# Optimization experiments

Hardware: AMD Instinct MI355X
Metric: run time of the kernel (lower is better)

## Reference

```python
import jax, jax.numpy as jnp
import numpy as np
from jax import lax

B, C, H, W = 32, 256, 56, 56
OUT_C, K, M = 256, 3, 8
STRIDE = (1, 1)
PADDING = ((1, 1), (1, 1))


def setup_inputs() -> dict:
    key = jax.random.key(0)
    ks = jax.random.split(key, 5)
    x = jax.random.normal(ks[0], (B, C, H, W), dtype=jnp.float32)
    # expert kernels: (M, out_C, in_C/groups, kh, kw), init like torch.randn*0.02
    weight = jax.random.normal(ks[1], (M, OUT_C, C, K, K), dtype=jnp.float32) * 0.02
    bias = jnp.zeros((M, OUT_C), dtype=jnp.float32)
    # gate Linear(in=C, out=M): torch stores weight as (out, in)
    bound = 1.0 / np.sqrt(C)
    gate_w = jax.random.uniform(ks[2], (M, C), minval=-bound, maxval=bound, dtype=jnp.float32)
    gate_b = jax.random.uniform(ks[3], (M,), minval=-bound, maxval=bound, dtype=jnp.float32)
    return {"x": x, "weight": weight, "bias": bias, "gate_w": gate_w, "gate_b": gate_b}


def reference(x, weight, bias, gate_w, gate_b):
    # global average pool -> gating
    gap = jnp.mean(x, axis=(2, 3))                         # (B, C)
    alpha = jax.nn.softmax(gap @ gate_w.T + gate_b, axis=1)  # (B, M)
    # per-sample combined kernels and biases
    kernels = jnp.einsum('bm,moikl->boikl', alpha, weight)  # (B, O, I, k, k)
    biases = alpha @ bias                                   # (B, O)

    def conv_one(xi, wi):
        # xi: (C,H,W), wi: (O,I,k,k)
        out = lax.conv_general_dilated(
            xi[None], wi,
            window_strides=STRIDE, padding=PADDING,
            dimension_numbers=('NCHW', 'OIHW', 'NCHW'))
        return out[0]  # (O, H, W)

    out = jax.vmap(conv_one)(x, kernels)                    # (B, O, H, W)
    return out + biases[:, :, None, None]
```

## Files before the change

### kernel.cpp

```cpp
#include <hip/hip_runtime.h>
#include <hip/hip_bf16.h>

#define B_    32
#define C_    256
#define HW_   3136
#define OC_   256
#define M_    8
#define KPB_  589824

typedef short v8s __attribute__((ext_vector_type(8)));
typedef float f32x4 __attribute__((ext_vector_type(4)));

union bf8pack { v8s v; __hip_bfloat16 h[8]; };

__device__ __forceinline__ void gll16(const short* src, short* dst) {
    __builtin_amdgcn_global_load_lds((const __attribute__((address_space(1))) void*)src,
                                     (__attribute__((address_space(3))) void*)dst, 16, 0, 0);
}

__global__ void zero_gap_kernel(float* __restrict__ gap) {
    gap[blockIdx.x * 256 + threadIdx.x] = 0.f;
}

__global__ __launch_bounds__(256) void xcast_kernel(const float* __restrict__ x,
                                                    short* __restrict__ xg,
                                                    float* __restrict__ gap) {
    __shared__ __hip_bfloat16 tile[64][65];
    int b = blockIdx.z, ct = blockIdx.y, pt = blockIdx.x;
    int p0 = pt*64, c0 = ct*64;
    int tp = threadIdx.x & 63, tc = threadIdx.x >> 6;
    const float* xb = x + ((size_t)b*C_ + c0) * HW_ + p0;
    #pragma unroll
    for (int j = 0; j < 16; ++j) {
        int cl = tc + j*4;
        float v = xb[(size_t)cl*HW_ + tp];
        tile[cl][tp] = __float2bfloat16(v);
        float s = v;
        #pragma unroll
        for (int off = 32; off; off >>= 1) s += __shfl_xor(s, off, 64);
        if (tp == 0) atomicAdd(&gap[b*C_ + c0 + cl], s);
    }
    __syncthreads();
    #pragma unroll
    for (int it = 0; it < 2; ++it) {
        int idx = it*256 + threadIdx.x;
        int px = idx >> 3, ck = idx & 7;
        bf8pack pk;
        #pragma unroll
        for (int j = 0; j < 8; ++j) pk.h[j] = tile[ck*8 + j][px];
        int c = c0 + ck*8;
        size_t dst = (((size_t)b*8 + (c >> 5))*HW_ + p0 + px)*32 + (c & 31);
        *(v8s*)(xg + dst) = pk.v;
    }
}

__global__ void alpha_kernel(const float* __restrict__ gap,
                             const float* __restrict__ gate_w,
                             const float* __restrict__ gate_b,
                             const float* __restrict__ bias,
                             float* __restrict__ alpha,
                             float* __restrict__ biasc) {
    int b = blockIdx.x, lane = threadIdx.x;
    const float inv = 1.0f / HW_;
    float g0 = gap[b*C_ + lane]*inv,       g1 = gap[b*C_ + 64 + lane]*inv;
    float g2 = gap[b*C_ + 128 + lane]*inv, g3 = gap[b*C_ + 192 + lane]*inv;
    float logit[M_];
    #pragma unroll
    for (int m = 0; m < M_; ++m) {
        const float* w = gate_w + m*C_;
        float s = g0*w[lane] + g1*w[64+lane] + g2*w[128+lane] + g3*w[192+lane];
        for (int off = 32; off; off >>= 1) s += __shfl_xor(s, off, 64);
        logit[m] = s + gate_b[m];
    }
    float mx = logit[0];
    #pragma unroll
    for (int m = 1; m < M_; ++m) mx = fmaxf(mx, logit[m]);
    float den = 0.f, e[M_];
    #pragma unroll
    for (int m = 0; m < M_; ++m) { e[m] = __expf(logit[m] - mx); den += e[m]; }
    float am[M_];
    #pragma unroll
    for (int m = 0; m < M_; ++m) am[m] = e[m] / den;
    if (lane < M_) alpha[b*M_ + lane] = am[lane];
    #pragma unroll
    for (int r = 0; r < 4; ++r) {
        int o = r*64 + lane;
        float s = 0.f;
        #pragma unroll
        for (int m = 0; m < M_; ++m) s += am[m] * bias[m*OC_ + o];
        biasc[b*OC_ + o] = s;
    }
}

__global__ __launch_bounds__(256) void combine_kernel(const float* __restrict__ weight,
                                                      const float* __restrict__ alpha,
                                                      short* __restrict__ wl) {
    __shared__ float as[B_*M_];
    as[threadIdx.x] = alpha[threadIdx.x];
    __syncthreads();
    int gc  = blockIdx.x*256 + threadIdx.x;
    int i8  = gc & 3;
    int o   = (gc >> 2) & 255;
    int t2  = gc >> 10;
    int tap = t2 % 9;
    int ib  = t2 / 9;
    int base = o*2304 + (ib*32 + i8*8)*9 + tap;
    float wv[M_][8];
    #pragma unroll
    for (int m = 0; m < M_; ++m)
        #pragma unroll
        for (int j = 0; j < 8; ++j)
            wv[m][j] = weight[(size_t)m*589824 + base + j*9];
    for (int b = 0; b < B_; ++b) {
        bf8pack pk;
        #pragma unroll
        for (int j = 0; j < 8; ++j) {
            float s = 0.f;
            #pragma unroll
            for (int m = 0; m < M_; ++m) s += as[b*M_+m] * wv[m][j];
            pk.h[j] = __float2bfloat16(s);
        }
        *(v8s*)(wl + (size_t)b*KPB_ + (size_t)gc*8) = pk.v;
    }
}

__global__ __launch_bounds__(256, 2) void conv_kernel(const short* __restrict__ xg,
                                                      const short* __restrict__ wl,
                                                      const float* __restrict__ biasc,
                                                      float* __restrict__ out) {
    __shared__ short smem[36864];

    const int wg  = blockIdx.x;
    const int swz = (wg & 7) * 104 + (wg >> 3);
    const int b   = swz / 26;
    const int rm  = swz - b * 26;
    const int ot  = rm / 13;
    const int pt  = rm - ot * 13;

    const int tid = threadIdx.x;
    const int wave = tid >> 6, lane = tid & 63, q = lane >> 4, ln = lane & 15;
    const int o_half = wave >> 1, p_half = wave & 1;
    const int P0 = pt*256;

    const int DOFF[9] = {-57,-56,-55,-1,0,1,55,56,57};

    unsigned vmask[8]; int p_lane[8];
    #pragma unroll
    for (int c = 0; c < 8; ++c) {
        int p = P0 + p_half*128 + c*16 + ln;
        p_lane[c] = p;
        int h = p/56, w = p%56;
        unsigned m = 0;
        #pragma unroll
        for (int tap = 0; tap < 9; ++tap) {
            int h2 = h + tap/3 - 1, w2 = w + tap%3 - 1;
            if ((unsigned)h2 < 56u && (unsigned)w2 < 56u) m |= (1u << tap);
        }
        vmask[c] = m;
    }

    const short* wbase = wl + (size_t)b*KPB_ + ot*4096 + tid*8;
    const short* xbase = xg + (size_t)(b*8)*HW_*32;

    auto stageA = [&](int kidx, int buf) {
        const short* src = wbase + (size_t)kidx*8192;
        gll16(src,        &smem[buf*4096 + tid*8]);
        gll16(src + 2048, &smem[buf*4096 + tid*8 + 2048]);
    };
    auto stageB = [&](int ib, int buf) {
        const short* src = xbase + ((long)ib*HW_ + P0 - 64)*32 + tid*8;
        short* dst = &smem[12288 + buf*12288 + tid*8];
        #pragma unroll
        for (int r = 0; r < 6; ++r) gll16(src + r*2048, dst + r*2048);
    };

    f32x4 acc[4][8];
    #pragma unroll
    for (int r = 0; r < 4; ++r)
        #pragma unroll
        for (int c = 0; c < 8; ++c) acc[r][c] = (f32x4){0.f,0.f,0.f,0.f};

    stageB(0, 0);
    stageA(0, 0);
    stageA(1, 1);

    const int a_lane_off = (o_half*64 + ln)*32 + q*8;
    const int b_lane_off = 12288 + (64 + p_half*128 + ln)*32 + q*8;
    const v8s vzero = {};

    for (int ib = 0; ib < 8; ++ib) {
        const short* bbuf = &smem[(ib & 1)*12288 + b_lane_off];
        #pragma unroll
        for (int tap = 0; tap < 9; ++tap) {
            const int k = ib*9 + tap;

            if (k == 71) {
                asm volatile("s_waitcnt vmcnt(0)" ::: "memory");
            } else if ((tap == 1 || tap == 2) && ib < 7) {
                asm volatile("s_waitcnt vmcnt(8)" ::: "memory");
            } else {
                asm volatile("s_waitcnt vmcnt(2)" ::: "memory");
            }
            __builtin_amdgcn_s_barrier();
            asm volatile("" ::: "memory");
            __builtin_amdgcn_sched_barrier(0);

            if (k + 2 < 72) stageA(k + 2, (tap + 2) % 3);
            if (tap == 0 && ib < 7) stageB(ib + 1, (ib + 1) & 1);

            const short* am = &smem[(tap % 3)*4096 + a_lane_off];
            v8s a[4];
            #pragma unroll
            for (int r = 0; r < 4; ++r) a[r] = *(const v8s*)(am + r*512);
            const short* bm = bbuf + DOFF[tap]*32;
            __builtin_amdgcn_s_setprio(1);
            #pragma unroll
            for (int c = 0; c < 8; ++c) {
                v8s v = *(const v8s*)(bm + c*512);
                v8s bf = ((vmask[c] >> tap) & 1) ? v : vzero;
                #pragma unroll
                for (int r = 0; r < 4; ++r)
                    acc[r][c] = __builtin_amdgcn_mfma_f32_16x16x32_bf16(a[r], bf, acc[r][c], 0, 0, 0);
            }
            __builtin_amdgcn_s_setprio(0);
        }
    }

    const int o_block = ot*128 + o_half*64;
    #pragma unroll
    for (int c = 0; c < 8; ++c) {
        int p = p_lane[c];
        if (p >= HW_) continue;
        float* op = out + (size_t)b * OC_ * HW_ + p;
        #pragma unroll
        for (int r = 0; r < 4; ++r) {
            int o0 = o_block + r*16 + q*4;
            #pragma unroll
            for (int reg = 0; reg < 4; ++reg) {
                int o = o0 + reg;
                op[(size_t)o * HW_] = acc[r][c][reg] + biasc[b*OC_ + o];
            }
        }
    }
}

extern "C" void kernel_launch(void* const* d_in, const int* in_sizes, int n_in,
                              void* d_out, int out_size, void* d_ws, size_t ws_size,
                              hipStream_t stream) {
    const float* x      = (const float*)d_in[0];
    const float* weight = (const float*)d_in[1];
    const float* bias   = (const float*)d_in[2];
    const float* gate_w = (const float*)d_in[3];
    const float* gate_b = (const float*)d_in[4];
    float* out = (float*)d_out;

    char* ws = (char*)d_ws;
    float* gap   = (float*)(ws);
    float* biasc = (float*)(ws + 32768);
    float* alpha = (float*)(ws + 65536);
    short* xg    = (short*)(ws + 131072);
    short* wl    = (short*)(ws + 51511296);

    zero_gap_kernel<<<32, 256, 0, stream>>>(gap);
    xcast_kernel   <<<dim3(49, 4, 32), 256, 0, stream>>>(x, xg, gap);
    alpha_kernel   <<<32,  64, 0, stream>>>(gap, gate_w, gate_b, bias, alpha, biasc);
    combine_kernel <<<288, 256, 0, stream>>>(weight, alpha, wl);
    conv_kernel    <<<832, 256, 0, stream>>>(xg, wl, biasc, out);
}
```

Measured before the change: 391.0 us.

## Enlarge conv tile to full 256 output channels by 224 pixels, split combine over batch

Each conv workgroup now covers all 256 output channels and 224 pixels (four pixel rows), where it used to cover 128 channels and 256 pixels. Weight reuse per staged input tile goes up, the padding waste at the end of the pixel range disappears, and the grid drops from 832 to 448 blocks with 1 block per CU. The combine kernel is also split across a second grid dimension over batch groups to add parallelism. In exchange, the larger accumulator array (56 f32x4) raises register pressure, occupancy is lower, and the wait counts were retuned by hand for the new load counts.

```diff
diff --git a/kernel.cpp b/kernel.cpp
--- a/kernel.cpp
+++ b/kernel.cpp
@@ -111,7 +111,8 @@
         #pragma unroll
         for (int j = 0; j < 8; ++j)
             wv[m][j] = weight[(size_t)m*589824 + base + j*9];
-    for (int b = 0; b < B_; ++b) {
+    int b0 = blockIdx.y * 8;
+    for (int b = b0; b < b0 + 8; ++b) {
         bf8pack pk;
         #pragma unroll
         for (int j = 0; j < 8; ++j) {
@@ -124,31 +125,27 @@
     }
 }
 
-__global__ __launch_bounds__(256, 2) void conv_kernel(const short* __restrict__ xg,
+__global__ __launch_bounds__(256, 1) void conv_kernel(const short* __restrict__ xg,
                                                       const short* __restrict__ wl,
                                                       const float* __restrict__ biasc,
                                                       float* __restrict__ out) {
-    __shared__ short smem[36864];
+    __shared__ short smem[49152];
 
     const int wg  = blockIdx.x;
-    const int swz = (wg & 7) * 104 + (wg >> 3);
-    const int b   = swz / 26;
-    const int rm  = swz - b * 26;
-    const int ot  = rm / 13;
-    const int pt  = rm - ot * 13;
+    const int swz = (wg & 7) * 56 + (wg >> 3);
+    const int b   = swz / 14;
+    const int pt  = swz - b * 14;
 
     const int tid = threadIdx.x;
     const int wave = tid >> 6, lane = tid & 63, q = lane >> 4, ln = lane & 15;
-    const int o_half = wave >> 1, p_half = wave & 1;
-    const int P0 = pt*256;
+    const int P0 = pt * 224;
 
     const int DOFF[9] = {-57,-56,-55,-1,0,1,55,56,57};
 
-    unsigned vmask[8]; int p_lane[8];
-    #pragma unroll
-    for (int c = 0; c < 8; ++c) {
-        int p = P0 + p_half*128 + c*16 + ln;
-        p_lane[c] = p;
+    unsigned vmask[14];
+    #pragma unroll
+    for (int c = 0; c < 14; ++c) {
+        int p = P0 + c*16 + ln;
         int h = p/56, w = p%56;
         unsigned m = 0;
         #pragma unroll
@@ -159,33 +156,34 @@
         vmask[c] = m;
     }
 
-    const short* wbase = wl + (size_t)b*KPB_ + ot*4096 + tid*8;
+    const short* wbase = wl + (size_t)b*KPB_ + tid*8;
     const short* xbase = xg + (size_t)(b*8)*HW_*32;
 
     auto stageA = [&](int kidx, int buf) {
         const short* src = wbase + (size_t)kidx*8192;
-        gll16(src,        &smem[buf*4096 + tid*8]);
-        gll16(src + 2048, &smem[buf*4096 + tid*8 + 2048]);
+        #pragma unroll
+        for (int r = 0; r < 4; ++r)
+            gll16(src + r*2048, &smem[buf*8192 + tid*8 + r*2048]);
     };
     auto stageB = [&](int ib, int buf) {
         const short* src = xbase + ((long)ib*HW_ + P0 - 64)*32 + tid*8;
-        short* dst = &smem[12288 + buf*12288 + tid*8];
+        short* dst = &smem[24576 + buf*12288 + tid*8];
         #pragma unroll
         for (int r = 0; r < 6; ++r) gll16(src + r*2048, dst + r*2048);
     };
 
-    f32x4 acc[4][8];
+    f32x4 acc[4][14];
     #pragma unroll
     for (int r = 0; r < 4; ++r)
         #pragma unroll
-        for (int c = 0; c < 8; ++c) acc[r][c] = (f32x4){0.f,0.f,0.f,0.f};
+        for (int c = 0; c < 14; ++c) acc[r][c] = (f32x4){0.f,0.f,0.f,0.f};
 
     stageB(0, 0);
     stageA(0, 0);
     stageA(1, 1);
 
-    const int a_lane_off = (o_half*64 + ln)*32 + q*8;
-    const int b_lane_off = 12288 + (64 + p_half*128 + ln)*32 + q*8;
+    const int a_lane_off = (wave*64 + ln)*32 + q*8;
+    const int b_lane_off = 24576 + (64 + ln)*32 + q*8;
     const v8s vzero = {};
 
     for (int ib = 0; ib < 8; ++ib) {
@@ -196,48 +194,44 @@
 
             if (k == 71) {
                 asm volatile("s_waitcnt vmcnt(0)" ::: "memory");
-            } else if ((tap == 1 || tap == 2) && ib < 7) {
-                asm volatile("s_waitcnt vmcnt(8)" ::: "memory");
+            } else if ((tap == 1 || tap == 2) && k <= 56) {
+                asm volatile("s_waitcnt vmcnt(10)" ::: "memory");
             } else {
-                asm volatile("s_waitcnt vmcnt(2)" ::: "memory");
+                asm volatile("s_waitcnt vmcnt(4)" ::: "memory");
             }
             __builtin_amdgcn_s_barrier();
             asm volatile("" ::: "memory");
             __builtin_amdgcn_sched_barrier(0);
 
-            if (k + 2 < 72) stageA(k + 2, (tap + 2) % 3);
+            if (k + 2 < 72) stageA(k + 2, (k + 2) % 3);
             if (tap == 0 && ib < 7) stageB(ib + 1, (ib + 1) & 1);
 
-            const short* am = &smem[(tap % 3)*4096 + a_lane_off];
+            const short* am = &smem[(k % 3)*8192 + a_lane_off];
             v8s a[4];
             #pragma unroll
             for (int r = 0; r < 4; ++r) a[r] = *(const v8s*)(am + r*512);
             const short* bm = bbuf + DOFF[tap]*32;
-            __builtin_amdgcn_s_setprio(1);
-            #pragma unroll
-            for (int c = 0; c < 8; ++c) {
+            #pragma unroll
+            for (int c = 0; c < 14; ++c) {
                 v8s v = *(const v8s*)(bm + c*512);
                 v8s bf = ((vmask[c] >> tap) & 1) ? v : vzero;
                 #pragma unroll
                 for (int r = 0; r < 4; ++r)
                     acc[r][c] = __builtin_amdgcn_mfma_f32_16x16x32_bf16(a[r], bf, acc[r][c], 0, 0, 0);
             }
-            __builtin_amdgcn_s_setprio(0);
-        }
-    }
-
-    const int o_block = ot*128 + o_half*64;
-    #pragma unroll
-    for (int c = 0; c < 8; ++c) {
-        int p = p_lane[c];
-        if (p >= HW_) continue;
+        }
+    }
+
+    const int o0 = wave*64 + q*4;
+    #pragma unroll
+    for (int c = 0; c < 14; ++c) {
+        int p = P0 + c*16 + ln;
         float* op = out + (size_t)b * OC_ * HW_ + p;
         #pragma unroll
         for (int r = 0; r < 4; ++r) {
-            int o0 = o_block + r*16 + q*4;
             #pragma unroll
             for (int reg = 0; reg < 4; ++reg) {
-                int o = o0 + reg;
+                int o = o0 + r*16 + reg;
                 op[(size_t)o * HW_] = acc[r][c][reg] + biasc[b*OC_ + o];
             }
         }
@@ -264,6 +258,6 @@
     zero_gap_kernel<<<32, 256, 0, stream>>>(gap);
     xcast_kernel   <<<dim3(49, 4, 32), 256, 0, stream>>>(x, xg, gap);
     alpha_kernel   <<<32,  64, 0, stream>>>(gap, gate_w, gate_b, bias, alpha, biasc);
-    combine_kernel <<<288, 256, 0, stream>>>(weight, alpha, wl);
-    conv_kernel    <<<832, 256, 0, stream>>>(xg, wl, biasc, out);
-}
+    combine_kernel <<<dim3(288, 4), 256, 0, stream>>>(weight, alpha, wl);
+    conv_kernel    <<<448, 256, 0, stream>>>(xg, wl, biasc, out);
+}
```

New measurement: 450.8 us. 15.3% more time.
